# Kernel tuning notes

Measured on AMD Instinct MI355X. Metric: run time of the kernel, lower is better.

The kernel has to match this reference:

```python
import jax, jax.numpy as jnp
import numpy as np

RATE = 0.001
B, IN, H1, H2, OUT, MH = 8, 1024, 1024, 1024, 512, 8


def setup_inputs() -> dict:
    key = jax.random.key(0)
    ks = jax.random.split(key, 9)
    s = 0.02  # small init so ReLU activations stay well-scaled
    return {
        "x":   jax.random.normal(ks[0], (B, IN), jnp.float32),
        "W1":  jax.random.normal(ks[1], (H1, IN), jnp.float32) * s,
        "b1":  jnp.zeros((H1,), jnp.float32),
        "W2":  jax.random.normal(ks[2], (H2, H1), jnp.float32) * s,
        "b2":  jnp.zeros((H2,), jnp.float32),
        "W3":  jax.random.normal(ks[3], (OUT, H2), jnp.float32) * s,
        "b3":  jnp.zeros((OUT,), jnp.float32),
        "cw1": jax.random.normal(ks[4], (MH, 3), jnp.float32) * 0.1,  # conv1 1x1 weight (out_ch, in_ch)
        "cb1": jnp.zeros((MH,), jnp.float32),
        "cw2": jax.random.normal(ks[5], (1, MH), jnp.float32) * 0.1,  # conv2 1x1 weight
        "cb2": jnp.zeros((1,), jnp.float32),
        "batch_num": 1,
    }


def _hebbian_layer(v, W, b, cw1, cb1, cw2, cb2, batch_num):
    # v: (B, i); W: (o, i)
    Bs, i = v.shape
    o = W.shape[0]
    vj = jax.nn.relu(v @ W.T + b)  # (B, o)
    # broadcast (vi, w, vj) triples to (B, o, i)
    vi_s = jnp.broadcast_to(v[:, None, :], (Bs, o, i))
    vj_s = jnp.broadcast_to(vj[:, :, None], (Bs, o, i))
    w_s  = jnp.broadcast_to(W[None, :, :], (Bs, o, i))
    meta = jnp.stack((vi_s, w_s, vj_s), axis=1)  # (B, 3, o, i) -- channel dim for 1x1 conv
    # conv1 (1x1, 3->MH) then conv2 (1x1, MH->1), no nonlinearity between (as in source)
    h = jnp.einsum('hc,bcoi->bhoi', cw1, meta) + cb1[None, :, None, None]  # (B, MH, o, i)
    shift = jnp.einsum('h,bhoi->boi', cw2[0], h) + cb2[0]                 # (B, o, i)
    shift = shift * (RATE / batch_num)
    return vj + jnp.sum(vi_s * shift, axis=2)  # (B, o)


def reference(x, W1, b1, W2, b2, W3, b3, cw1, cb1, cw2, cb2, batch_num):
    out = _hebbian_layer(x,   W1, b1, cw1, cb1, cw2, cb2, batch_num)
    out = _hebbian_layer(out, W2, b2, cw1, cb1, cw2, cb2, batch_num)
    out = _hebbian_layer(out, W3, b3, cw1, cb1, cw2, cb2, batch_num)
    return out
```

## Files before the change

### kernel.cpp

```cpp
#include <hip/hip_runtime.h>


#define RATE_F 0.001f

__global__ __launch_bounds__(256) void hebb_layer(
    const float* __restrict__ vin,
    const float* __restrict__ W,
    const float* __restrict__ bias,
    const float* __restrict__ cw1,
    const float* __restrict__ cb1,
    const float* __restrict__ cw2,
    const float* __restrict__ cb2,
    const int*   __restrict__ batch_num,
    float*       __restrict__ vout,
    int n_out)
{
    constexpr int NIN = 1024;
    constexpr int BATCH = 8;
    __shared__ float vsh[BATCH * NIN];
    __shared__ float coeff[8];
    __shared__ float svs[BATCH], s2s[BATCH];

    const int tid  = threadIdx.x;
    const int w    = tid >> 6, lane = tid & 63;
    const int o    = blockIdx.x * 4 + w;

    const float4* Wrow = (const float4*)(W + (size_t)o * NIN);
    const int i0a = lane * 8;
    const int i0b = 512 + lane * 8;
    const float4 w0 = Wrow[(i0a >> 2) + 0];
    const float4 w1 = Wrow[(i0a >> 2) + 1];
    const float4 w2 = Wrow[(i0b >> 2) + 0];
    const float4 w3 = Wrow[(i0b >> 2) + 1];
    const float  bo = bias[o];

    {
        const float4* p = (const float4*)vin;
        for (int k = tid; k < 2048; k += 256) {
            *(float4*)&vsh[k * 4] = p[k];
        }
    }

    if (tid == 0) {
        float a0 = 0.f, a1 = 0.f, a2 = 0.f, cc = 0.f;
        #pragma unroll
        for (int h = 0; h < 8; h++) {
            float c2 = cw2[h];
            a0 += c2 * cw1[h * 3 + 0];
            a1 += c2 * cw1[h * 3 + 1];
            a2 += c2 * cw1[h * 3 + 2];
            cc += c2 * cb1[h];
        }
        cc += cb2[0];
        coeff[0] = a0; coeff[1] = a1; coeff[2] = a2; coeff[3] = cc;
        coeff[4] = RATE_F / (float)batch_num[0];
    }
    __syncthreads();

    {
        int b = tid >> 5, j = tid & 31;
        float sv = 0.f, s2 = 0.f;
        for (int i = j; i < NIN; i += 32) {
            float v = vsh[b * NIN + i];
            sv += v; s2 += v * v;
        }
        #pragma unroll
        for (int m = 16; m >= 1; m >>= 1) {
            sv += __shfl_xor(sv, m, 64);
            s2 += __shfl_xor(s2, m, 64);
        }
        if (j == 0) { svs[b] = sv; s2s[b] = s2; }
    }
    __syncthreads();

    float acc[BATCH] = {0.f, 0.f, 0.f, 0.f, 0.f, 0.f, 0.f, 0.f};
    #pragma unroll
    for (int b = 0; b < BATCH; b++) {
        const float4 v0 = *(const float4*)&vsh[b * NIN + i0a];
        const float4 v1 = *(const float4*)&vsh[b * NIN + i0a + 4];
        const float4 v2 = *(const float4*)&vsh[b * NIN + i0b];
        const float4 v3 = *(const float4*)&vsh[b * NIN + i0b + 4];
        acc[b] += w0.x * v0.x + w0.y * v0.y + w0.z * v0.z + w0.w * v0.w
                + w1.x * v1.x + w1.y * v1.y + w1.z * v1.z + w1.w * v1.w
                + w2.x * v2.x + w2.y * v2.y + w2.z * v2.z + w2.w * v2.w
                + w3.x * v3.x + w3.y * v3.y + w3.z * v3.z + w3.w * v3.w;
    }
    #pragma unroll
    for (int b = 0; b < BATCH; b++) {
        #pragma unroll
        for (int m = 32; m >= 1; m >>= 1)
            acc[b] += __shfl_xor(acc[b], m, 64);
    }

    if (lane < BATCH) {
        const int b = lane;
        const float dot = acc[b];
        float vj = dot + bo;
        vj = vj > 0.f ? vj : 0.f;
        const float r = coeff[4];
        const float outv = vj + r * (coeff[0] * s2s[b] + coeff[1] * dot
                                     + (coeff[2] * vj + coeff[3]) * svs[b]);
        vout[(size_t)b * n_out + o] = outv;
    }
}

extern "C" void kernel_launch(void* const* d_in, const int* in_sizes, int n_in,
                              void* d_out, int out_size, void* d_ws, size_t ws_size,
                              hipStream_t stream) {
    const float* x   = (const float*)d_in[0];
    const float* W1  = (const float*)d_in[1];
    const float* b1  = (const float*)d_in[2];
    const float* W2  = (const float*)d_in[3];
    const float* b2  = (const float*)d_in[4];
    const float* W3  = (const float*)d_in[5];
    const float* b3  = (const float*)d_in[6];
    const float* cw1 = (const float*)d_in[7];
    const float* cb1 = (const float*)d_in[8];
    const float* cw2 = (const float*)d_in[9];
    const float* cb2 = (const float*)d_in[10];
    const int*   bn  = (const int*)d_in[11];

    float* v1 = (float*)d_ws;
    float* v2 = v1 + 8 * 1024;

    hebb_layer<<<256, 256, 0, stream>>>(x,  W1, b1, cw1, cb1, cw2, cb2, bn, v1, 1024);
    hebb_layer<<<256, 256, 0, stream>>>(v1, W2, b2, cw1, cb1, cw2, cb2, bn, v2, 1024);
    hebb_layer<<<128, 256, 0, stream>>>(v2, W3, b3, cw1, cb1, cw2, cb2, bn, (float*)d_out, 512);
}
```

Measured before the change: 101.2 us.

## Fuse three Hebbian layers into one cooperative kernel with grid syncs

Replaces three separate layer launches with a single cooperative launch of 256 blocks that runs all three layers, separated by a thread fence and grid.sync. The mixing coefficients are now computed once per block instead of once per layer. This is meant to remove the launch gaps and kernel-boundary overhead between the dependent layers. The cost is the grid-wide barriers, plus the third layer now uses only 2 of 4 waves per block.

```diff
diff --git a/kernel.cpp b/kernel.cpp
--- a/kernel.cpp
+++ b/kernel.cpp
@@ -1,59 +1,48 @@
 #include <hip/hip_runtime.h>
+#include <hip/hip_cooperative_groups.h>
+
+namespace cg = cooperative_groups;
 
 
 #define RATE_F 0.001f
+constexpr int NIN   = 1024;
+constexpr int BATCH = 8;
 
-__global__ __launch_bounds__(256) void hebb_layer(
+struct Smem {
+    float vsh[BATCH * NIN];
+    float coeff[8];
+    float svs[BATCH], s2s[BATCH];
+};
+
+__device__ __forceinline__ void hebb_phase(
     const float* __restrict__ vin,
     const float* __restrict__ W,
     const float* __restrict__ bias,
-    const float* __restrict__ cw1,
-    const float* __restrict__ cb1,
-    const float* __restrict__ cw2,
-    const float* __restrict__ cb2,
-    const int*   __restrict__ batch_num,
     float*       __restrict__ vout,
-    int n_out)
+    int n_out, int rpb, Smem& sm)
 {
-    constexpr int NIN = 1024;
-    constexpr int BATCH = 8;
-    __shared__ float vsh[BATCH * NIN];
-    __shared__ float coeff[8];
-    __shared__ float svs[BATCH], s2s[BATCH];
-
     const int tid  = threadIdx.x;
     const int w    = tid >> 6, lane = tid & 63;
-    const int o    = blockIdx.x * 4 + w;
+    const int o    = blockIdx.x * rpb + w;
+    const bool active = (w < rpb);
 
-    const float4* Wrow = (const float4*)(W + (size_t)o * NIN);
     const int i0a = lane * 8;
     const int i0b = 512 + lane * 8;
-    const float4 w0 = Wrow[(i0a >> 2) + 0];
-    const float4 w1 = Wrow[(i0a >> 2) + 1];
-    const float4 w2 = Wrow[(i0b >> 2) + 0];
-    const float4 w3 = Wrow[(i0b >> 2) + 1];
-    const float  bo = bias[o];
+    float4 w0, w1, w2, w3;
+    float  bo = 0.f;
+    if (active) {
+        const float4* Wrow = (const float4*)(W + (size_t)o * NIN);
+        w0 = Wrow[(i0a >> 2) + 0];
+        w1 = Wrow[(i0a >> 2) + 1];
+        w2 = Wrow[(i0b >> 2) + 0];
+        w3 = Wrow[(i0b >> 2) + 1];
+        bo = bias[o];
+    }
 
     {
         const float4* p = (const float4*)vin;
-        for (int k = tid; k < 2048; k += 256) {
-            *(float4*)&vsh[k * 4] = p[k];
-        }
-    }
-
-    if (tid == 0) {
-        float a0 = 0.f, a1 = 0.f, a2 = 0.f, cc = 0.f;
-        #pragma unroll
-        for (int h = 0; h < 8; h++) {
-            float c2 = cw2[h];
-            a0 += c2 * cw1[h * 3 + 0];
-            a1 += c2 * cw1[h * 3 + 1];
-            a2 += c2 * cw1[h * 3 + 2];
-            cc += c2 * cb1[h];
-        }
-        cc += cb2[0];
-        coeff[0] = a0; coeff[1] = a1; coeff[2] = a2; coeff[3] = cc;
-        coeff[4] = RATE_F / (float)batch_num[0];
+        for (int k = tid; k < 2048; k += 256)
+            *(float4*)&sm.vsh[k * 4] = p[k];
     }
     __syncthreads();
 
@@ -61,7 +50,7 @@
         int b = tid >> 5, j = tid & 31;
         float sv = 0.f, s2 = 0.f;
         for (int i = j; i < NIN; i += 32) {
-            float v = vsh[b * NIN + i];
+            float v = sm.vsh[b * NIN + i];
             sv += v; s2 += v * v;
         }
         #pragma unroll
@@ -69,17 +58,19 @@
             sv += __shfl_xor(sv, m, 64);
             s2 += __shfl_xor(s2, m, 64);
         }
-        if (j == 0) { svs[b] = sv; s2s[b] = s2; }
+        if (j == 0) { sm.svs[b] = sv; sm.s2s[b] = s2; }
     }
     __syncthreads();
+
+    if (!active) return;
 
     float acc[BATCH] = {0.f, 0.f, 0.f, 0.f, 0.f, 0.f, 0.f, 0.f};
     #pragma unroll
     for (int b = 0; b < BATCH; b++) {
-        const float4 v0 = *(const float4*)&vsh[b * NIN + i0a];
-        const float4 v1 = *(const float4*)&vsh[b * NIN + i0a + 4];
-        const float4 v2 = *(const float4*)&vsh[b * NIN + i0b];
-        const float4 v3 = *(const float4*)&vsh[b * NIN + i0b + 4];
+        const float4 v0 = *(const float4*)&sm.vsh[b * NIN + i0a];
+        const float4 v1 = *(const float4*)&sm.vsh[b * NIN + i0a + 4];
+        const float4 v2 = *(const float4*)&sm.vsh[b * NIN + i0b];
+        const float4 v3 = *(const float4*)&sm.vsh[b * NIN + i0b + 4];
         acc[b] += w0.x * v0.x + w0.y * v0.y + w0.z * v0.z + w0.w * v0.w
                 + w1.x * v1.x + w1.y * v1.y + w1.z * v1.z + w1.w * v1.w
                 + w2.x * v2.x + w2.y * v2.y + w2.z * v2.z + w2.w * v2.w
@@ -97,11 +88,49 @@
         const float dot = acc[b];
         float vj = dot + bo;
         vj = vj > 0.f ? vj : 0.f;
-        const float r = coeff[4];
-        const float outv = vj + r * (coeff[0] * s2s[b] + coeff[1] * dot
-                                     + (coeff[2] * vj + coeff[3]) * svs[b]);
+        const float r = sm.coeff[4];
+        const float outv = vj + r * (sm.coeff[0] * sm.s2s[b] + sm.coeff[1] * dot
+                                     + (sm.coeff[2] * vj + sm.coeff[3]) * sm.svs[b]);
         vout[(size_t)b * n_out + o] = outv;
     }
+}
+
+__global__ __launch_bounds__(256, 1) void hebb_fused(
+    const float* __restrict__ x,
+    const float* __restrict__ W1, const float* __restrict__ b1,
+    const float* __restrict__ W2, const float* __restrict__ b2,
+    const float* __restrict__ W3, const float* __restrict__ b3,
+    const float* __restrict__ cw1, const float* __restrict__ cb1,
+    const float* __restrict__ cw2, const float* __restrict__ cb2,
+    const int*   __restrict__ batch_num,
+    float* __restrict__ v1, float* __restrict__ v2,
+    float* __restrict__ out)
+{
+    __shared__ Smem sm;
+    cg::grid_group grid = cg::this_grid();
+
+    if (threadIdx.x == 0) {
+        float a0 = 0.f, a1 = 0.f, a2 = 0.f, cc = 0.f;
+        #pragma unroll
+        for (int h = 0; h < 8; h++) {
+            float c2 = cw2[h];
+            a0 += c2 * cw1[h * 3 + 0];
+            a1 += c2 * cw1[h * 3 + 1];
+            a2 += c2 * cw1[h * 3 + 2];
+            cc += c2 * cb1[h];
+        }
+        cc += cb2[0];
+        sm.coeff[0] = a0; sm.coeff[1] = a1; sm.coeff[2] = a2; sm.coeff[3] = cc;
+        sm.coeff[4] = RATE_F / (float)batch_num[0];
+    }
+
+    hebb_phase(x,  W1, b1, v1,  1024, 4, sm);
+    __threadfence();
+    grid.sync();
+    hebb_phase(v1, W2, b2, v2,  1024, 4, sm);
+    __threadfence();
+    grid.sync();
+    hebb_phase(v2, W3, b3, out,  512, 2, sm);
 }
 
 extern "C" void kernel_launch(void* const* d_in, const int* in_sizes, int n_in,
@@ -120,10 +149,14 @@
     const float* cb2 = (const float*)d_in[10];
     const int*   bn  = (const int*)d_in[11];
 
-    float* v1 = (float*)d_ws;
-    float* v2 = v1 + 8 * 1024;
+    float* v1  = (float*)d_ws;
+    float* v2  = v1 + 8 * 1024;
+    float* out = (float*)d_out;
 
-    hebb_layer<<<256, 256, 0, stream>>>(x,  W1, b1, cw1, cb1, cw2, cb2, bn, v1, 1024);
-    hebb_layer<<<256, 256, 0, stream>>>(v1, W2, b2, cw1, cb1, cw2, cb2, bn, v2, 1024);
-    hebb_layer<<<128, 256, 0, stream>>>(v2, W3, b3, cw1, cb1, cw2, cb2, bn, (float*)d_out, 512);
+    void* args[] = { (void*)&x, (void*)&W1, (void*)&b1, (void*)&W2, (void*)&b2,
+                     (void*)&W3, (void*)&b3, (void*)&cw1, (void*)&cb1,
+                     (void*)&cw2, (void*)&cb2, (void*)&bn,
+                     (void*)&v1, (void*)&v2, (void*)&out };
+    hipLaunchCooperativeKernel((void*)hebb_fused, dim3(256), dim3(256),
+                               args, 0, stream);
 }
```

After: 209.6 us. 107% more time.

## Drop shared-memory staging; read activations directly and compute stats per wave

Applied to the files above, without the earlier changes.

Removes the 32KB shared-memory staging of the input activations and both block barriers. Each wave now reads its slice of the activations from global/L2 and computes the per-batch sum and sum of squares alongside the dot product, reducing everything with wave shuffles. The mixing coefficients are computed redundantly per thread instead of by one thread through shared memory. This trades LDS capacity and barrier stalls (and higher occupancy) for three times as many shuffle reductions and repeated L2 reads of the activation vector per wave.

```diff
diff --git a/kernel.cpp b/kernel.cpp
--- a/kernel.cpp
+++ b/kernel.cpp
@@ -15,92 +15,67 @@
     float*       __restrict__ vout,
     int n_out)
 {
-    constexpr int NIN = 1024;
-    constexpr int BATCH = 8;
-    __shared__ float vsh[BATCH * NIN];
-    __shared__ float coeff[8];
-    __shared__ float svs[BATCH], s2s[BATCH];
+    const int tid  = threadIdx.x;
+    const int lane = tid & 63;
+    const int o    = blockIdx.x * 4 + (tid >> 6);
 
-    const int tid  = threadIdx.x;
-    const int w    = tid >> 6, lane = tid & 63;
-    const int o    = blockIdx.x * 4 + w;
-
-    const float4* Wrow = (const float4*)(W + (size_t)o * NIN);
-    const int i0a = lane * 8;
-    const int i0b = 512 + lane * 8;
-    const float4 w0 = Wrow[(i0a >> 2) + 0];
-    const float4 w1 = Wrow[(i0a >> 2) + 1];
-    const float4 w2 = Wrow[(i0b >> 2) + 0];
-    const float4 w3 = Wrow[(i0b >> 2) + 1];
+    const float4* Wrow = (const float4*)(W + (size_t)o * 1024);
+    const int ia = lane * 2;
+    const int ib = 128 + lane * 2;
+    const float4 w0 = Wrow[ia], w1 = Wrow[ia + 1];
+    const float4 w2 = Wrow[ib], w3 = Wrow[ib + 1];
     const float  bo = bias[o];
 
-    {
-        const float4* p = (const float4*)vin;
-        for (int k = tid; k < 2048; k += 256) {
-            *(float4*)&vsh[k * 4] = p[k];
+    float a0 = 0.f, a1 = 0.f, a2 = 0.f, cc = 0.f;
+    #pragma unroll
+    for (int h = 0; h < 8; h++) {
+        const float c2 = cw2[h];
+        a0 += c2 * cw1[h * 3 + 0];
+        a1 += c2 * cw1[h * 3 + 1];
+        a2 += c2 * cw1[h * 3 + 2];
+        cc += c2 * cb1[h];
+    }
+    cc += cb2[0];
+    const float r = RATE_F / (float)batch_num[0];
+
+    const float4* v4 = (const float4*)vin;
+    float acc[8], sv[8], s2[8];
+    #pragma unroll
+    for (int b = 0; b < 8; b++) {
+        const float4 v0 = v4[b * 256 + ia], v1 = v4[b * 256 + ia + 1];
+        const float4 v2 = v4[b * 256 + ib], v3 = v4[b * 256 + ib + 1];
+        acc[b] = w0.x * v0.x + w0.y * v0.y + w0.z * v0.z + w0.w * v0.w
+               + w1.x * v1.x + w1.y * v1.y + w1.z * v1.z + w1.w * v1.w
+               + w2.x * v2.x + w2.y * v2.y + w2.z * v2.z + w2.w * v2.w
+               + w3.x * v3.x + w3.y * v3.y + w3.z * v3.z + w3.w * v3.w;
+        sv[b]  = v0.x + v0.y + v0.z + v0.w + v1.x + v1.y + v1.z + v1.w
+               + v2.x + v2.y + v2.z + v2.w + v3.x + v3.y + v3.z + v3.w;
+        s2[b]  = v0.x * v0.x + v0.y * v0.y + v0.z * v0.z + v0.w * v0.w
+               + v1.x * v1.x + v1.y * v1.y + v1.z * v1.z + v1.w * v1.w
+               + v2.x * v2.x + v2.y * v2.y + v2.z * v2.z + v2.w * v2.w
+               + v3.x * v3.x + v3.y * v3.y + v3.z * v3.z + v3.w * v3.w;
+    }
+
+    #pragma unroll
+    for (int b = 0; b < 8; b++) {
+        #pragma unroll
+        for (int m = 32; m >= 1; m >>= 1) {
+            acc[b] += __shfl_xor(acc[b], m, 64);
+            sv[b]  += __shfl_xor(sv[b],  m, 64);
+            s2[b]  += __shfl_xor(s2[b],  m, 64);
         }
     }
 
-    if (tid == 0) {
-        float a0 = 0.f, a1 = 0.f, a2 = 0.f, cc = 0.f;
+    if (lane < 8) {
+        float dot = 0.f, svv = 0.f, s2v = 0.f;
         #pragma unroll
-        for (int h = 0; h < 8; h++) {
-            float c2 = cw2[h];
-            a0 += c2 * cw1[h * 3 + 0];
-            a1 += c2 * cw1[h * 3 + 1];
-            a2 += c2 * cw1[h * 3 + 2];
-            cc += c2 * cb1[h];
-        }
-        cc += cb2[0];
-        coeff[0] = a0; coeff[1] = a1; coeff[2] = a2; coeff[3] = cc;
-        coeff[4] = RATE_F / (float)batch_num[0];
-    }
-    __syncthreads();
-
-    {
-        int b = tid >> 5, j = tid & 31;
-        float sv = 0.f, s2 = 0.f;
-        for (int i = j; i < NIN; i += 32) {
-            float v = vsh[b * NIN + i];
-            sv += v; s2 += v * v;
-        }
-        #pragma unroll
-        for (int m = 16; m >= 1; m >>= 1) {
-            sv += __shfl_xor(sv, m, 64);
-            s2 += __shfl_xor(s2, m, 64);
-        }
-        if (j == 0) { svs[b] = sv; s2s[b] = s2; }
-    }
-    __syncthreads();
-
-    float acc[BATCH] = {0.f, 0.f, 0.f, 0.f, 0.f, 0.f, 0.f, 0.f};
-    #pragma unroll
-    for (int b = 0; b < BATCH; b++) {
-        const float4 v0 = *(const float4*)&vsh[b * NIN + i0a];
-        const float4 v1 = *(const float4*)&vsh[b * NIN + i0a + 4];
-        const float4 v2 = *(const float4*)&vsh[b * NIN + i0b];
-        const float4 v3 = *(const float4*)&vsh[b * NIN + i0b + 4];
-        acc[b] += w0.x * v0.x + w0.y * v0.y + w0.z * v0.z + w0.w * v0.w
-                + w1.x * v1.x + w1.y * v1.y + w1.z * v1.z + w1.w * v1.w
-                + w2.x * v2.x + w2.y * v2.y + w2.z * v2.z + w2.w * v2.w
-                + w3.x * v3.x + w3.y * v3.y + w3.z * v3.z + w3.w * v3.w;
-    }
-    #pragma unroll
-    for (int b = 0; b < BATCH; b++) {
-        #pragma unroll
-        for (int m = 32; m >= 1; m >>= 1)
-            acc[b] += __shfl_xor(acc[b], m, 64);
-    }
-
-    if (lane < BATCH) {
-        const int b = lane;
-        const float dot = acc[b];
+        for (int b = 0; b < 8; b++)
+            if (lane == b) { dot = acc[b]; svv = sv[b]; s2v = s2[b]; }
         float vj = dot + bo;
         vj = vj > 0.f ? vj : 0.f;
-        const float r = coeff[4];
-        const float outv = vj + r * (coeff[0] * s2s[b] + coeff[1] * dot
-                                     + (coeff[2] * vj + coeff[3]) * svs[b]);
-        vout[(size_t)b * n_out + o] = outv;
+        const float outv = vj + r * (a0 * s2v + a1 * dot
+                                     + (a2 * vj + cc) * svv);
+        vout[(size_t)lane * n_out + o] = outv;
     }
 }
 
```

Result: no change. 100.1 us (-1.1%).
